# Performance work log

Measured on AMD Instinct MI355X. Metric: run time of the kernel, lower is better.

The kernel has to match this reference:

```python
import jax, jax.numpy as jnp
import numpy as np
import math

D_MODEL, N_HEADS, D_HEAD, D_MLP = 768, 12, 64, 3072
EPS = 1e-5
IGNORE = -100000.0


def _ln(x, w, b):
    mu = jnp.mean(x, axis=-1, keepdims=True)
    xc = x - mu
    scale = jnp.sqrt(jnp.mean(xc * xc, axis=-1, keepdims=True) + EPS)
    return (xc / scale) * w + b


def _gelu_new(x):
    # GPT-2 'new' gelu
    return 0.5 * x * (1.0 + jnp.tanh(jnp.sqrt(2.0 / jnp.pi) * (x + 0.044715 * x ** 3)))


def setup_inputs() -> dict:
    key = jax.random.key(0)
    ks = jax.random.split(key, 12)
    std = 0.02
    inp = {
        "resid_pre": jax.random.normal(ks[0], (8, 1024, D_MODEL), jnp.float32),
        "W_Q": jax.random.normal(ks[1], (N_HEADS, D_MODEL, D_HEAD), jnp.float32) * std,
        "b_Q": jnp.zeros((N_HEADS, D_HEAD), jnp.float32),
        "W_K": jax.random.normal(ks[2], (N_HEADS, D_MODEL, D_HEAD), jnp.float32) * std,
        "b_K": jnp.zeros((N_HEADS, D_HEAD), jnp.float32),
        "W_V": jax.random.normal(ks[3], (N_HEADS, D_MODEL, D_HEAD), jnp.float32) * std,
        "b_V": jnp.zeros((N_HEADS, D_HEAD), jnp.float32),
        "W_O": jax.random.normal(ks[4], (N_HEADS, D_HEAD, D_MODEL), jnp.float32) * std,
        "b_O": jnp.zeros((D_MODEL,), jnp.float32),
        "ln1_w": jnp.ones((D_MODEL,), jnp.float32),
        "ln1_b": jnp.zeros((D_MODEL,), jnp.float32),
        "ln2_w": jnp.ones((D_MODEL,), jnp.float32),
        "ln2_b": jnp.zeros((D_MODEL,), jnp.float32),
        "W_in": jax.random.normal(ks[5], (D_MODEL, D_MLP), jnp.float32) * std,
        "b_in": jnp.zeros((D_MLP,), jnp.float32),
        "W_out": jax.random.normal(ks[6], (D_MLP, D_MODEL), jnp.float32) * std,
        "b_out": jnp.zeros((D_MODEL,), jnp.float32),
    }
    return inp


def reference(resid_pre, W_Q, b_Q, W_K, b_K, W_V, b_V, W_O, b_O,
              ln1_w, ln1_b, ln2_w, ln2_b, W_in, b_in, W_out, b_out):
    # ---- ln1 + attention ----
    n = _ln(resid_pre, ln1_w, ln1_b)  # [b, s, d]; broadcast over heads in einsums
    q = jnp.einsum('bsd,hde->bshe', n, W_Q) + b_Q
    k = jnp.einsum('bsd,hde->bshe', n, W_K) + b_K
    v = jnp.einsum('bsd,hde->bshe', n, W_V) + b_V
    scores = jnp.einsum('bqhe,bkhe->bhqk', q, k) / math.sqrt(D_HEAD)
    S = scores.shape[-1]
    causal = jnp.triu(jnp.ones((S, S), dtype=bool), k=1)
    scores = jnp.where(causal, IGNORE, scores)
    pattern = jax.nn.softmax(scores, axis=-1)
    z = jnp.einsum('bhqk,bkhe->bqhe', pattern, v)
    # per-head output with b_O / n_heads each (as in source), then summed over heads
    attn_per_head = jnp.einsum('bqhe,hed->bqhd', z, W_O) + b_O / N_HEADS
    attn_out = attn_per_head.sum(axis=2)  # [b, s, d]
    resid_mid = resid_pre + attn_out
    # ---- ln2 + mlp ----
    n2 = _ln(resid_mid, ln2_w, ln2_b)
    pre = jnp.einsum('bsd,dm->bsm', n2, W_in) + b_in
    post = _gelu_new(pre)
    mlp_out = jnp.einsum('bsm,md->bsd', post, W_out) + b_out
    return resid_mid + mlp_out
```

## Files before the change

kernel.cpp:

```cpp
#include <hip/hip_runtime.h>
#include <hip/hip_bf16.h>

typedef unsigned short u16;
typedef float f32x4 __attribute__((ext_vector_type(4)));
typedef __bf16 bf16x8 __attribute__((ext_vector_type(8)));
typedef unsigned short u16x8 __attribute__((ext_vector_type(8)));
typedef unsigned short u16x4 __attribute__((ext_vector_type(4)));

__device__ __forceinline__ float b2f(u16 u) {
    unsigned v = ((unsigned)u) << 16;
    return __builtin_bit_cast(float, v);
}
__device__ __forceinline__ u16 f2b(float f) {
    unsigned u = __builtin_bit_cast(unsigned, f);
    u += 0x7fffu + ((u >> 16) & 1u);
    return (u16)(u >> 16);
}
__device__ __forceinline__ bf16x8 ldfrag(const u16* p) {
    return __builtin_bit_cast(bf16x8, *(const u16x8*)p);
}
__device__ __forceinline__ f32x4 mfma16(bf16x8 a, bf16x8 b, f32x4 c) {
    return __builtin_amdgcn_mfma_f32_16x16x32_bf16(a, b, c, 0, 0, 0);
}
__device__ __forceinline__ void gload_lds16(const u16* g, u16* l) {
    __builtin_amdgcn_global_load_lds(
        (const __attribute__((address_space(1))) unsigned int*)(g),
        (__attribute__((address_space(3))) unsigned int*)(l), 16, 0, 0);
}

#define T_TOK 8192
#define DM 768
#define NH 12
#define DH 64
#define DMLP 3072
#define SEQ 1024
#define QKV_LD 2304
#define QK_LD 1536

#define OFF_WQKV ((size_t)0)
#define OFF_WO   (OFF_WQKV + (size_t)2304*768)
#define OFF_WIN  (OFF_WO   + (size_t)768*768)
#define OFF_WOUT (OFF_WIN  + (size_t)768*3072)
#define OFF_BQKV (OFF_WOUT + (size_t)3072*768)
#define P0       (OFF_BQKV + (size_t)4608)

#define SZ_N    ((size_t)T_TOK*DM)
#define SZ_QKV  ((size_t)T_TOK*QKV_LD)
#define A_NBUF   (P0)
#define A_QKV    (P0 + SZ_N)
#define A_Z      (P0 + SZ_N + SZ_QKV)
#define A_N2     (P0)
#define A_POST   (P0 + SZ_N)
#define PATHA_BYTES (((size_t)(P0 + SZ_N + SZ_QKV + SZ_N)) * 2)
#define B_Z      (P0)
#define B_QKVB   (P0 + SZ_N)
#define B_NBUF   (B_QKVB + (size_t)SEQ*QKV_LD)
#define B_N2     (P0)
#define B_POSTC  (P0 + SZ_N)

#define PR0 (2304*768)
#define PR1 (768*768)
#define PR2 (768*3072)
#define PR3 (3072*768)
#define PREP_TOTAL (PR0+PR1+PR2+PR3+2304)

__global__ __launch_bounds__(256) void prep_kernel(
    const float* __restrict__ WQ, const float* __restrict__ WK, const float* __restrict__ WV,
    const float* __restrict__ WO, const float* __restrict__ Win, const float* __restrict__ Wout,
    const float* __restrict__ bQ, const float* __restrict__ bK, const float* __restrict__ bV,
    u16* __restrict__ Wqkv_t, u16* __restrict__ Wo_t, u16* __restrict__ Win_t,
    u16* __restrict__ Wout_t, float* __restrict__ bias_qkv)
{
    int idx = blockIdx.x * 256 + threadIdx.x;
    if (idx < PR0) {
        int r = idx / 768, d = idx % 768;
        int which = r / 768;
        int he = r % 768;
        int h = he >> 6, e = he & 63;
        const float* W = (which == 0) ? WQ : ((which == 1) ? WK : WV);
        Wqkv_t[idx] = f2b(W[h * 49152 + d * 64 + e]);
    } else if (idx < PR0 + PR1) {
        int o = idx - PR0;
        int d = o / 768, he = o % 768;
        Wo_t[o] = f2b(WO[he * 768 + d]);
    } else if (idx < PR0 + PR1 + PR2) {
        int o = idx - PR0 - PR1;
        int m = o / 768, d = o % 768;
        Win_t[o] = f2b(Win[d * 3072 + m]);
    } else if (idx < PR0 + PR1 + PR2 + PR3) {
        int o = idx - PR0 - PR1 - PR2;
        int d = o / 3072, m = o % 3072;
        Wout_t[o] = f2b(Wout[m * 768 + d]);
    } else if (idx < PREP_TOTAL) {
        int j = idx - (PR0 + PR1 + PR2 + PR3);
        bias_qkv[j] = (j < 768) ? bQ[j] : ((j < 1536) ? bK[j - 768] : bV[j - 1536]);
    }
}

__global__ __launch_bounds__(256) void ln_kernel(
    const float* __restrict__ x, const float* __restrict__ w,
    const float* __restrict__ bb, u16* __restrict__ out)
{
    __shared__ float red[4];
    size_t base = (size_t)blockIdx.x * DM;
    int tid = threadIdx.x;
    float v0 = x[base + tid], v1 = x[base + tid + 256], v2 = x[base + tid + 512];
    float s = v0 + v1 + v2;
#pragma unroll
    for (int off = 32; off > 0; off >>= 1) s += __shfl_xor(s, off);
    if ((tid & 63) == 0) red[tid >> 6] = s;
    __syncthreads();
    float mu = (red[0] + red[1] + red[2] + red[3]) * (1.0f / 768.0f);
    v0 -= mu; v1 -= mu; v2 -= mu;
    float q = v0 * v0 + v1 * v1 + v2 * v2;
    __syncthreads();
#pragma unroll
    for (int off = 32; off > 0; off >>= 1) q += __shfl_xor(q, off);
    if ((tid & 63) == 0) red[tid >> 6] = q;
    __syncthreads();
    float var = (red[0] + red[1] + red[2] + red[3]) * (1.0f / 768.0f);
    float sc = rsqrtf(var + 1e-5f);
    out[base + tid]       = f2b(v0 * sc * w[tid]       + bb[tid]);
    out[base + tid + 256] = f2b(v1 * sc * w[tid + 256] + bb[tid + 256]);
    out[base + tid + 512] = f2b(v2 * sc * w[tid + 512] + bb[tid + 512]);
}

template <int EPI>
__global__ __launch_bounds__(256) void gemm_bt_kernel(
    const u16* __restrict__ A, const u16* __restrict__ BT,
    const float* __restrict__ bias, const float* __restrict__ aux,
    void* __restrict__ outp, int N, int K)
{
    __shared__ __align__(16) u16 As[128 * 32];
    __shared__ __align__(16) u16 Bs[128 * 32];
    const int tid = threadIdx.x;
    const int w = tid >> 6, l = tid & 63;
    const int lr = l & 15, lq = l >> 4;
    const int bm = blockIdx.x * 128, bn = blockIdx.y * 128;
    const int wm = (w >> 1) * 64, wn = (w & 1) * 64;

    f32x4 acc[4][4];
#pragma unroll
    for (int i = 0; i < 4; i++)
#pragma unroll
        for (int j = 0; j < 4; j++) acc[i][j] = f32x4{0.f, 0.f, 0.f, 0.f};

    const int srow = w * 32 + (l >> 2);
    const int scol = (l & 3) * 8;
    const u16* Ab = A  + (size_t)(bm + srow) * K + scol;
    const u16* Bb = BT + (size_t)(bn + srow) * K + scol;
    u16* AsD = As + w * 1024;
    u16* BsD = Bs + w * 1024;

    const int kiter = K >> 5;
    for (int kk = 0; kk < kiter; ++kk) {
        const int k0 = kk * 32;
        gload_lds16(Ab + k0,          AsD);
        gload_lds16(Ab + 16 * K + k0, AsD + 512);
        gload_lds16(Bb + k0,          BsD);
        gload_lds16(Bb + 16 * K + k0, BsD + 512);
        __syncthreads();
        bf16x8 af[4], bf[4];
#pragma unroll
        for (int mt = 0; mt < 4; mt++) af[mt] = ldfrag(&As[(wm + mt * 16 + lr) * 32 + lq * 8]);
#pragma unroll
        for (int nt = 0; nt < 4; nt++) bf[nt] = ldfrag(&Bs[(wn + nt * 16 + lr) * 32 + lq * 8]);
#pragma unroll
        for (int mt = 0; mt < 4; mt++)
#pragma unroll
            for (int nt = 0; nt < 4; nt++)
                acc[mt][nt] = mfma16(af[mt], bf[nt], acc[mt][nt]);
        __syncthreads();
    }

    if (EPI == 4) {
        const bool isv = (bn >= 1536);
        u16* vtg = (u16*)aux;
#pragma unroll
        for (int mt = 0; mt < 4; mt++) {
            int row0 = bm + wm + mt * 16 + lq * 4;
            if (!isv) {
#pragma unroll
                for (int r = 0; r < 4; r++) {
                    size_t ro = (size_t)(row0 + r) * QK_LD;
#pragma unroll
                    for (int nt = 0; nt < 4; nt++) {
                        int col = bn + wn + nt * 16 + lr;
                        ((u16*)outp)[ro + col] = f2b(acc[mt][nt][r] + bias[col]);
                    }
                }
            } else {
                int bloc = row0 >> 10;
                int s = row0 & 1023;
#pragma unroll
                for (int nt = 0; nt < 4; nt++) {
                    int col = bn + wn + nt * 16 + lr;
                    int he = col - 1536;
                    float bcol = bias[col];
                    u16x4 pk;
                    pk[0] = f2b(acc[mt][nt][0] + bcol);
                    pk[1] = f2b(acc[mt][nt][1] + bcol);
                    pk[2] = f2b(acc[mt][nt][2] + bcol);
                    pk[3] = f2b(acc[mt][nt][3] + bcol);
                    *(u16x4*)&vtg[(size_t)bloc * (NH * 64 * SEQ)
                                  + (size_t)he * SEQ + s] = pk;
                }
            }
        }
        return;
    }

#pragma unroll
    for (int mt = 0; mt < 4; mt++) {
#pragma unroll
        for (int r = 0; r < 4; r++) {
            int row = bm + wm + mt * 16 + lq * 4 + r;
            size_t ro = (size_t)row * N;
#pragma unroll
            for (int nt = 0; nt < 4; nt++) {
                int col = bn + wn + nt * 16 + lr;
                float v = acc[mt][nt][r] + bias[col];
                if (EPI == 0) {
                    ((u16*)outp)[ro + col] = f2b(v);
                } else if (EPI == 1) {
                    ((float*)outp)[ro + col] = v + aux[ro + col];
                } else if (EPI == 2) {
                    float x = v;
                    float t = tanhf(0.7978845608028654f * (x + 0.044715f * x * x * x));
                    ((u16*)outp)[ro + col] = f2b(0.5f * x * (1.0f + t));
                } else {
                    ((float*)outp)[ro + col] = v + aux[ro + col];
                }
            }
        }
    }
}

__global__ __launch_bounds__(256, 5) void attn_kernel(
    const u16* __restrict__ qk, const u16* __restrict__ vtg,
    u16* __restrict__ z, int b0, int bq0)
{
    __shared__ __align__(16) u16 Ks[64 * 72];
    __shared__ __align__(16) u16 Vt[64 * 72];
    __shared__ __align__(16) u16 Ps[4][16 * 72];

    const int qt = (int)(gridDim.x - 1) - (int)blockIdx.x;
    const int bh = blockIdx.y;
    const int b = b0 + bh / NH, h = bh % NH;
    const int tid = threadIdx.x, w = tid >> 6, l = tid & 63;
    const int lr = l & 15, lq = l >> 4;
    const int qbase = qt * 64;
    const u16* qp = qk + (size_t)(b - bq0) * SEQ * QK_LD + h * 64;
    const u16* kp = qp + 768;
    const u16* vthead = vtg + ((size_t)(b - bq0) * NH + h) * (64 * SEQ);
    u16* PsW = &Ps[w][0];

    bf16x8 aq0, aq1;
    {
        const u16* qrow = qp + (size_t)(qbase + w * 16 + lr) * QK_LD + lq * 8;
        aq0 = ldfrag(qrow);
        aq1 = ldfrag(qrow + 32);
    }

    float m_i = -1e30f;
    float l_i = 0.f;
    f32x4 O[4];
#pragma unroll
    for (int i = 0; i < 4; i++) O[i] = f32x4{0.f, 0.f, 0.f, 0.f};

    const int nkt = qt + 1;
    const int srow = tid >> 2;
    const int spart = (tid & 3) * 16;

    u16x8 kreg0, kreg1, vreg0, vreg1;
    {
        const u16* ks = kp + (size_t)srow * QK_LD + spart;
        kreg0 = *(const u16x8*)ks;
        kreg1 = *(const u16x8*)(ks + 8);
        const u16* vs = vthead + (size_t)srow * SEQ + spart;
        vreg0 = *(const u16x8*)vs;
        vreg1 = *(const u16x8*)(vs + 8);
    }

    for (int kt = 0; kt < nkt; ++kt) {
        __syncthreads();
        *(u16x8*)&Ks[srow * 72 + spart]     = kreg0;
        *(u16x8*)&Ks[srow * 72 + spart + 8] = kreg1;
        *(u16x8*)&Vt[srow * 72 + spart]     = vreg0;
        *(u16x8*)&Vt[srow * 72 + spart + 8] = vreg1;
        __syncthreads();
        if (kt + 1 < nkt) {
            const u16* ks = kp + (size_t)((kt + 1) * 64 + srow) * QK_LD + spart;
            kreg0 = *(const u16x8*)ks;
            kreg1 = *(const u16x8*)(ks + 8);
            const u16* vs = vthead + (size_t)srow * SEQ + (kt + 1) * 64 + spart;
            vreg0 = *(const u16x8*)vs;
            vreg1 = *(const u16x8*)(vs + 8);
        }

        f32x4 S[4];
#pragma unroll
        for (int nt = 0; nt < 4; nt++) S[nt] = f32x4{0.f, 0.f, 0.f, 0.f};
#pragma unroll
        for (int nt = 0; nt < 4; nt++) {
            bf16x8 bk0 = ldfrag(&Ks[(nt * 16 + lr) * 72 + lq * 8]);
            bf16x8 bk1 = ldfrag(&Ks[(nt * 16 + lr) * 72 + 32 + lq * 8]);
            S[nt] = mfma16(bk0, aq0, S[nt]);
            S[nt] = mfma16(bk1, aq1, S[nt]);
        }

        const bool diag = (kt == qt);
        float mx = -1e30f;
#pragma unroll
        for (int nt = 0; nt < 4; nt++)
#pragma unroll
            for (int r = 0; r < 4; r++) {
                float sv = S[nt][r] * 0.125f;
                if (diag) sv = (nt * 16 + lq * 4 + r <= w * 16 + lr) ? sv : -1e30f;
                S[nt][r] = sv;
                mx = fmaxf(mx, sv);
            }
        mx = fmaxf(mx, __shfl_xor(mx, 16));
        mx = fmaxf(mx, __shfl_xor(mx, 32));
        float mn = fmaxf(m_i, mx);
        float alpha = __expf(m_i - mn);
        m_i = mn;
        float rs = 0.f;
#pragma unroll
        for (int nt = 0; nt < 4; nt++) {
            u16x4 pk;
#pragma unroll
            for (int r = 0; r < 4; r++) {
                float pe = __expf(S[nt][r] - mn);
                rs += pe;
                pk[r] = f2b(pe);
            }
            *(u16x4*)&PsW[lr * 72 + nt * 16 + lq * 4] = pk;
        }
        rs += __shfl_xor(rs, 16);
        rs += __shfl_xor(rs, 32);
        l_i = l_i * alpha + rs;

#pragma unroll
        for (int r = 0; r < 4; r++) {
            float ar = __shfl(alpha, (l & 48) | (lq * 4 + r));
            O[0][r] *= ar; O[1][r] *= ar; O[2][r] *= ar; O[3][r] *= ar;
        }

#pragma unroll
        for (int kq = 0; kq < 2; kq++) {
            bf16x8 ap = ldfrag(&PsW[lr * 72 + kq * 32 + lq * 8]);
#pragma unroll
            for (int ot = 0; ot < 4; ot++) {
                bf16x8 bv = ldfrag(&Vt[(ot * 16 + lr) * 72 + kq * 32 + lq * 8]);
                O[ot] = mfma16(ap, bv, O[ot]);
            }
        }
    }

    float li[4];
#pragma unroll
    for (int r = 0; r < 4; r++)
        li[r] = __shfl(l_i, (l & 48) | (lq * 4 + r));
#pragma unroll
    for (int ot = 0; ot < 4; ot++)
#pragma unroll
        for (int r = 0; r < 4; r++) {
            int q = qbase + w * 16 + lq * 4 + r;
            size_t t = (size_t)b * SEQ + q;
            z[t * DM + h * 64 + ot * 16 + lr] = f2b(O[ot][r] / li[r]);
        }
}

extern "C" void kernel_launch(void* const* d_in, const int* in_sizes, int n_in,
                              void* d_out, int out_size, void* d_ws, size_t ws_size,
                              hipStream_t stream) {
    const float* resid_pre = (const float*)d_in[0];
    const float* W_Q  = (const float*)d_in[1];
    const float* b_Q  = (const float*)d_in[2];
    const float* W_K  = (const float*)d_in[3];
    const float* b_K  = (const float*)d_in[4];
    const float* W_V  = (const float*)d_in[5];
    const float* b_V  = (const float*)d_in[6];
    const float* W_O  = (const float*)d_in[7];
    const float* b_O  = (const float*)d_in[8];
    const float* ln1w = (const float*)d_in[9];
    const float* ln1b = (const float*)d_in[10];
    const float* ln2w = (const float*)d_in[11];
    const float* ln2b = (const float*)d_in[12];
    const float* W_in  = (const float*)d_in[13];
    const float* b_in  = (const float*)d_in[14];
    const float* W_out = (const float*)d_in[15];
    const float* b_out = (const float*)d_in[16];

    u16* ws16       = (u16*)d_ws;
    u16* Wqkv_t     = ws16 + OFF_WQKV;
    u16* Wo_t       = ws16 + OFF_WO;
    u16* Win_t      = ws16 + OFF_WIN;
    u16* Wout_t     = ws16 + OFF_WOUT;
    float* bias_qkv = (float*)(ws16 + OFF_BQKV);
    float* outp  = (float*)d_out;
    float* resid = (float*)d_out;

    prep_kernel<<<(PREP_TOTAL + 255) / 256, 256, 0, stream>>>(
        W_Q, W_K, W_V, W_O, W_in, W_out, b_Q, b_K, b_V,
        Wqkv_t, Wo_t, Win_t, Wout_t, bias_qkv);

    if (ws_size >= PATHA_BYTES) {
        u16* nbuf    = ws16 + A_NBUF;
        u16* qkbuf   = ws16 + A_QKV;
        u16* vtgA    = ws16 + A_QKV + (size_t)T_TOK * QK_LD;
        u16* zbuf    = ws16 + A_Z;
        u16* n2buf   = ws16 + A_N2;
        u16* postbuf = ws16 + A_POST;

        ln_kernel<<<T_TOK, 256, 0, stream>>>(resid_pre, ln1w, ln1b, nbuf);
        gemm_bt_kernel<4><<<dim3(T_TOK / 128, QKV_LD / 128), 256, 0, stream>>>(
            nbuf, Wqkv_t, bias_qkv, (const float*)vtgA, qkbuf, QKV_LD, DM);
        attn_kernel<<<dim3(SEQ / 64, 8 * NH), 256, 0, stream>>>(qkbuf, vtgA, zbuf, 0, 0);
        gemm_bt_kernel<1><<<dim3(T_TOK / 128, DM / 128), 256, 0, stream>>>(
            zbuf, Wo_t, b_O, resid_pre, resid, DM, DM);
        ln_kernel<<<T_TOK, 256, 0, stream>>>(resid, ln2w, ln2b, n2buf);
        gemm_bt_kernel<2><<<dim3(T_TOK / 128, DMLP / 128), 256, 0, stream>>>(
            n2buf, Win_t, b_in, nullptr, postbuf, DMLP, DM);
        gemm_bt_kernel<3><<<dim3(T_TOK / 128, DM / 128), 256, 0, stream>>>(
            postbuf, Wout_t, b_out, resid, outp, DM, DMLP);
    } else {
        u16* zbuf   = ws16 + B_Z;
        u16* qkb    = ws16 + B_QKVB;
        u16* vtgB   = qkb + (size_t)SEQ * QK_LD;
        u16* nbuf   = ws16 + B_NBUF;
        u16* n2buf  = ws16 + B_N2;
        u16* postc  = ws16 + B_POSTC;

        ln_kernel<<<T_TOK, 256, 0, stream>>>(resid_pre, ln1w, ln1b, nbuf);
        for (int b = 0; b < 8; b++) {
            gemm_bt_kernel<4><<<dim3(SEQ / 128, QKV_LD / 128), 256, 0, stream>>>(
                nbuf + (size_t)b * SEQ * DM, Wqkv_t, bias_qkv, (const float*)vtgB, qkb, QKV_LD, DM);
            attn_kernel<<<dim3(SEQ / 64, NH), 256, 0, stream>>>(qkb, vtgB, zbuf, b, b);
        }
        gemm_bt_kernel<1><<<dim3(T_TOK / 128, DM / 128), 256, 0, stream>>>(
            zbuf, Wo_t, b_O, resid_pre, resid, DM, DM);
        ln_kernel<<<T_TOK, 256, 0, stream>>>(resid, ln2w, ln2b, n2buf);
        for (int c = 0; c < 4; c++) {
            const size_t r0 = (size_t)c * 2048;
            gemm_bt_kernel<2><<<dim3(2048 / 128, DMLP / 128), 256, 0, stream>>>(
                n2buf + r0 * DM, Win_t, b_in, nullptr, postc, DMLP, DM);
            gemm_bt_kernel<3><<<dim3(2048 / 128, DM / 128), 256, 0, stream>>>(
                postc, Wout_t, b_out, resid + r0 * DM, outp + r0 * DM, DM, DMLP);
        }
    }
}
```

Before: 450.4 us.

## Add 64-row GEMM tiles for N=768 GEMMs, XOR-swizzle LDS, faster GELU

Templates the GEMM on the M tile size and launches the two N=768 GEMMs (attention output projection and MLP down-projection) with 64-row tiles, doubling their block count so more of the GPU's compute units stay busy. Adds an XOR swizzle on the 16-byte chunk index for both the global-to-LDS writes and the fragment reads, to reduce LDS bank conflicts. Rewrites the tanh-based GELU as x/(1+exp(-2y)), which is algebraically equal and cheaper to evaluate. The smaller tiles lower data reuse per block, and the exp form can differ slightly in rounding.

```diff
diff --git a/kernel.cpp b/kernel.cpp
--- a/kernel.cpp
+++ b/kernel.cpp
@@ -125,48 +125,51 @@
     out[base + tid + 512] = f2b(v2 * sc * w[tid + 512] + bb[tid + 512]);
 }
 
-template <int EPI>
+template <int EPI, int TM>
 __global__ __launch_bounds__(256) void gemm_bt_kernel(
     const u16* __restrict__ A, const u16* __restrict__ BT,
     const float* __restrict__ bias, const float* __restrict__ aux,
     void* __restrict__ outp, int N, int K)
 {
-    __shared__ __align__(16) u16 As[128 * 32];
+    __shared__ __align__(16) u16 As[TM * 32];
     __shared__ __align__(16) u16 Bs[128 * 32];
     const int tid = threadIdx.x;
     const int w = tid >> 6, l = tid & 63;
     const int lr = l & 15, lq = l >> 4;
-    const int bm = blockIdx.x * 128, bn = blockIdx.y * 128;
-    const int wm = (w >> 1) * 64, wn = (w & 1) * 64;
-
-    f32x4 acc[4][4];
-#pragma unroll
-    for (int i = 0; i < 4; i++)
+    const int bm = blockIdx.x * TM, bn = blockIdx.y * 128;
+    constexpr int MT = TM / 32;
+    const int wm = (w >> 1) * (TM / 2), wn = (w & 1) * 64;
+
+    f32x4 acc[MT][4];
+#pragma unroll
+    for (int i = 0; i < MT; i++)
 #pragma unroll
         for (int j = 0; j < 4; j++) acc[i][j] = f32x4{0.f, 0.f, 0.f, 0.f};
 
-    const int srow = w * 32 + (l >> 2);
-    const int scol = (l & 3) * 8;
-    const u16* Ab = A  + (size_t)(bm + srow) * K + scol;
-    const u16* Bb = BT + (size_t)(bn + srow) * K + scol;
-    u16* AsD = As + w * 1024;
+    const int srow_a = (TM == 128) ? (w * 32 + (l >> 2)) : (w * 16 + (l >> 2));
+    const int srow_b = w * 32 + (l >> 2);
+    const int scol = ((l & 3) ^ ((l >> 2) & 3)) * 8;
+    const u16* Ab = A  + (size_t)(bm + srow_a) * K + scol;
+    const u16* Bb = BT + (size_t)(bn + srow_b) * K + scol;
+    u16* AsD = As + ((TM == 128) ? w * 1024 : w * 512);
     u16* BsD = Bs + w * 1024;
+    const int rchunk = (lq ^ (lr & 3)) * 8;
 
     const int kiter = K >> 5;
     for (int kk = 0; kk < kiter; ++kk) {
         const int k0 = kk * 32;
-        gload_lds16(Ab + k0,          AsD);
-        gload_lds16(Ab + 16 * K + k0, AsD + 512);
+        gload_lds16(Ab + k0, AsD);
+        if (TM == 128) gload_lds16(Ab + 16 * K + k0, AsD + 512);
         gload_lds16(Bb + k0,          BsD);
         gload_lds16(Bb + 16 * K + k0, BsD + 512);
         __syncthreads();
-        bf16x8 af[4], bf[4];
-#pragma unroll
-        for (int mt = 0; mt < 4; mt++) af[mt] = ldfrag(&As[(wm + mt * 16 + lr) * 32 + lq * 8]);
-#pragma unroll
-        for (int nt = 0; nt < 4; nt++) bf[nt] = ldfrag(&Bs[(wn + nt * 16 + lr) * 32 + lq * 8]);
-#pragma unroll
-        for (int mt = 0; mt < 4; mt++)
+        bf16x8 af[MT], bf[4];
+#pragma unroll
+        for (int mt = 0; mt < MT; mt++) af[mt] = ldfrag(&As[(wm + mt * 16 + lr) * 32 + rchunk]);
+#pragma unroll
+        for (int nt = 0; nt < 4; nt++) bf[nt] = ldfrag(&Bs[(wn + nt * 16 + lr) * 32 + rchunk]);
+#pragma unroll
+        for (int mt = 0; mt < MT; mt++)
 #pragma unroll
             for (int nt = 0; nt < 4; nt++)
                 acc[mt][nt] = mfma16(af[mt], bf[nt], acc[mt][nt]);
@@ -177,7 +180,7 @@
         const bool isv = (bn >= 1536);
         u16* vtg = (u16*)aux;
 #pragma unroll
-        for (int mt = 0; mt < 4; mt++) {
+        for (int mt = 0; mt < MT; mt++) {
             int row0 = bm + wm + mt * 16 + lq * 4;
             if (!isv) {
 #pragma unroll
@@ -211,7 +214,7 @@
     }
 
 #pragma unroll
-    for (int mt = 0; mt < 4; mt++) {
+    for (int mt = 0; mt < MT; mt++) {
 #pragma unroll
         for (int r = 0; r < 4; r++) {
             int row = bm + wm + mt * 16 + lq * 4 + r;
@@ -226,8 +229,8 @@
                     ((float*)outp)[ro + col] = v + aux[ro + col];
                 } else if (EPI == 2) {
                     float x = v;
-                    float t = tanhf(0.7978845608028654f * (x + 0.044715f * x * x * x));
-                    ((u16*)outp)[ro + col] = f2b(0.5f * x * (1.0f + t));
+                    float y = 0.7978845608028654f * (x + 0.044715f * x * x * x);
+                    ((u16*)outp)[ro + col] = f2b(x / (1.0f + __expf(-2.0f * y)));
                 } else {
                     ((float*)outp)[ro + col] = v + aux[ro + col];
                 }
@@ -415,15 +418,15 @@
         u16* postbuf = ws16 + A_POST;
 
         ln_kernel<<<T_TOK, 256, 0, stream>>>(resid_pre, ln1w, ln1b, nbuf);
-        gemm_bt_kernel<4><<<dim3(T_TOK / 128, QKV_LD / 128), 256, 0, stream>>>(
+        gemm_bt_kernel<4, 128><<<dim3(T_TOK / 128, QKV_LD / 128), 256, 0, stream>>>(
             nbuf, Wqkv_t, bias_qkv, (const float*)vtgA, qkbuf, QKV_LD, DM);
         attn_kernel<<<dim3(SEQ / 64, 8 * NH), 256, 0, stream>>>(qkbuf, vtgA, zbuf, 0, 0);
-        gemm_bt_kernel<1><<<dim3(T_TOK / 128, DM / 128), 256, 0, stream>>>(
+        gemm_bt_kernel<1, 64><<<dim3(T_TOK / 64, DM / 128), 256, 0, stream>>>(
             zbuf, Wo_t, b_O, resid_pre, resid, DM, DM);
         ln_kernel<<<T_TOK, 256, 0, stream>>>(resid, ln2w, ln2b, n2buf);
-        gemm_bt_kernel<2><<<dim3(T_TOK / 128, DMLP / 128), 256, 0, stream>>>(
+        gemm_bt_kernel<2, 128><<<dim3(T_TOK / 128, DMLP / 128), 256, 0, stream>>>(
             n2buf, Win_t, b_in, nullptr, postbuf, DMLP, DM);
-        gemm_bt_kernel<3><<<dim3(T_TOK / 128, DM / 128), 256, 0, stream>>>(
+        gemm_bt_kernel<3, 64><<<dim3(T_TOK / 64, DM / 128), 256, 0, stream>>>(
             postbuf, Wout_t, b_out, resid, outp, DM, DMLP);
     } else {
         u16* zbuf   = ws16 + B_Z;
@@ -435,18 +438,18 @@
 
         ln_kernel<<<T_TOK, 256, 0, stream>>>(resid_pre, ln1w, ln1b, nbuf);
         for (int b = 0; b < 8; b++) {
-            gemm_bt_kernel<4><<<dim3(SEQ / 128, QKV_LD / 128), 256, 0, stream>>>(
+            gemm_bt_kernel<4, 128><<<dim3(SEQ / 128, QKV_LD / 128), 256, 0, stream>>>(
                 nbuf + (size_t)b * SEQ * DM, Wqkv_t, bias_qkv, (const float*)vtgB, qkb, QKV_LD, DM);
             attn_kernel<<<dim3(SEQ / 64, NH), 256, 0, stream>>>(qkb, vtgB, zbuf, b, b);
         }
-        gemm_bt_kernel<1><<<dim3(T_TOK / 128, DM / 128), 256, 0, stream>>>(
+        gemm_bt_kernel<1, 64><<<dim3(T_TOK / 64, DM / 128), 256, 0, stream>>>(
             zbuf, Wo_t, b_O, resid_pre, resid, DM, DM);
         ln_kernel<<<T_TOK, 256, 0, stream>>>(resid, ln2w, ln2b, n2buf);
         for (int c = 0; c < 4; c++) {
             const size_t r0 = (size_t)c * 2048;
-            gemm_bt_kernel<2><<<dim3(2048 / 128, DMLP / 128), 256, 0, stream>>>(
+            gemm_bt_kernel<2, 128><<<dim3(2048 / 128, DMLP / 128), 256, 0, stream>>>(
                 n2buf + r0 * DM, Win_t, b_in, nullptr, postc, DMLP, DM);
-            gemm_bt_kernel<3><<<dim3(2048 / 128, DM / 128), 256, 0, stream>>>(
+            gemm_bt_kernel<3, 64><<<dim3(2048 / 64, DM / 128), 256, 0, stream>>>(
                 postc, Wout_t, b_out, resid + r0 * DM, outp + r0 * DM, DM, DMLP);
         }
     }
```

Result: faster. 440.9 us (-2.1%).
